# Kernel optimization log

Hardware: AMD Instinct MI355X
Metric: run time of the kernel (lower is better)

Reference implementation:

```python
import jax, jax.numpy as jnp
import numpy as np

HIDDEN = 1024
HEADS = 16
HEAD_DIM = HIDDEN // HEADS  # 64
RP_DIM = 256
KERNEL_EPS = 1e-3


def _gaussian_orthogonal_matrix(nb_rows, nb_cols, seed=0):
    """Orthogonal random features (scaling=0), as in Performer FAVOR+."""
    rng = np.random.RandomState(seed)
    blocks = []
    n_full = nb_rows // nb_cols
    for _ in range(n_full):
        q, _ = np.linalg.qr(rng.randn(nb_cols, nb_cols))
        blocks.append(q.T)
    rem = nb_rows - n_full * nb_cols
    if rem > 0:
        q, _ = np.linalg.qr(rng.randn(nb_cols, nb_cols))
        blocks.append(q.T[:rem])
    mat = np.concatenate(blocks, axis=0)
    # scaling=0: row norms drawn from chi distribution (norms of gaussian rows)
    multiplier = np.linalg.norm(rng.randn(nb_rows, nb_cols), axis=1)
    return (multiplier[:, None] * mat).astype(np.float32)


def setup_inputs() -> dict:
    key = jax.random.key(0)
    kx, kw = jax.random.split(key)
    x = jax.random.normal(kx, (4, 4096, HIDDEN), dtype=jnp.float32)
    w_qkv = jax.random.normal(kw, (HIDDEN, 3 * HIDDEN), dtype=jnp.float32) * 0.02
    b_qkv = jnp.zeros((3 * HIDDEN,), dtype=jnp.float32)
    proj = jnp.asarray(_gaussian_orthogonal_matrix(RP_DIM, HEAD_DIM))  # [M, Dh]
    return {"x": x, "w_qkv": w_qkv, "b_qkv": b_qkv, "proj": proj}


def reference(x, w_qkv, b_qkv, proj):
    B, N, _ = x.shape
    qkv = x @ w_qkv + b_qkv  # [B, N, 3*hidden]
    q, k, v = jnp.split(qkv, 3, axis=-1)

    def to_heads(t):
        return t.reshape(B, N, HEADS, HEAD_DIM).transpose(0, 2, 1, 3)  # bhnd

    q, k, v = to_heads(q), to_heads(k), to_heads(v)

    # forward scales by d**-0.25, generalized_kernel normalizes by d**-0.25 again
    scale = HEAD_DIM ** -0.5
    # generalized kernel features: relu(x_norm @ proj^T) + eps  -> [B,H,N,M]
    q_prime = jax.nn.relu(jnp.einsum('bhnd,md->bhnm', q * scale, proj)) + KERNEL_EPS
    k_prime = jax.nn.relu(jnp.einsum('bhnd,md->bhnm', k * scale, proj)) + KERNEL_EPS

    # non-causal linear attention
    k_sum = k_prime.sum(axis=2)  # [B,H,M]
    d_inv = 1.0 / jnp.einsum('bhnm,bhm->bhn', q_prime, k_sum)  # [B,H,N]
    context = jnp.einsum('bhnm,bhnd->bhmd', k_prime, v)  # [B,H,M,Dh]
    out = jnp.einsum('bhmd,bhnm,bhn->bhnd', context, q_prime, d_inv)

    out = out.transpose(0, 2, 1, 3).reshape(B, N, HIDDEN)
    return out
```

## Files before the change

kernel.cpp:

```cpp
#include <hip/hip_runtime.h>

#define B_   4
#define N_   4096
#define NH   16
#define DH   64
#define HID  1024
#define NC3  3072
#define M_   256
#define BH   64
#define SCALE 0.125f
#define EPS   1e-3f
#define CH2  8
#define CH3  8

typedef _Float16 half8  __attribute__((ext_vector_type(8)));
typedef _Float16 half4v __attribute__((ext_vector_type(4)));
typedef float floatx4   __attribute__((ext_vector_type(4)));

#define GLD_LDS16(gptr, lds_base) \
  __builtin_amdgcn_global_load_lds((const __attribute__((address_space(1))) void*)(gptr), \
                                   (__attribute__((address_space(3))) void*)(lds_base), 16, 0, 0)

#define SBAR() asm volatile("s_barrier" ::: "memory")

__global__ __launch_bounds__(256) void convert_xh(
    const float* __restrict__ x, _Float16* __restrict__ xh,
    const float* __restrict__ proj, _Float16* __restrict__ projh)
{
    if (blockIdx.x >= 8192) {
        const int i = (blockIdx.x - 8192) * 256 + threadIdx.x;
        projh[i] = (_Float16)proj[i];
        return;
    }
    const size_t i = ((size_t)blockIdx.x * 256 + threadIdx.x) * 8;
    float4 a = *(const float4*)(x + i);
    float4 b = *(const float4*)(x + i + 4);
    half8 h;
    h[0] = (_Float16)a.x; h[1] = (_Float16)a.y; h[2] = (_Float16)a.z; h[3] = (_Float16)a.w;
    h[4] = (_Float16)b.x; h[5] = (_Float16)b.y; h[6] = (_Float16)b.z; h[7] = (_Float16)b.w;
    *(half8*)(xh + i) = h;
}

__global__ __launch_bounds__(256) void convert_wT(
    const float* __restrict__ w, _Float16* __restrict__ wT)
{
    __shared__ float t[64][65];
    const int tid = threadIdx.x;
    const int kb = blockIdx.y * 64, nb = blockIdx.x * 64;
    const int c = tid & 63, r0 = tid >> 6;
#pragma unroll
    for (int rr = 0; rr < 64; rr += 4)
        t[rr + r0][c] = w[(size_t)(kb + rr + r0) * NC3 + nb + c];
    __syncthreads();
    const float sc = (nb < 2048) ? SCALE : 1.0f;
#pragma unroll
    for (int rr = 0; rr < 64; rr += 4)
        wT[(size_t)(nb + rr + r0) * HID + kb + c] = (_Float16)(t[c][rr + r0] * sc);
}

__device__ __forceinline__ void stage_tile_qkv(
    const _Float16* __restrict__ xh, const _Float16* __restrict__ wT,
    int row0, int col0, int kt, char* ab, char* bb, int wv, int srow, int sblk)
{
    const size_t ko = (size_t)kt * 64;
#pragma unroll
    for (int s = 0; s < 4; ++s) {
        const int r = s * 64 + srow;
        GLD_LDS16(xh + (size_t)(row0 + r) * HID + ko + 8 * sblk, ab + s * 8192 + wv * 1024);
        GLD_LDS16(wT + (size_t)(col0 + r) * HID + ko + 8 * sblk, bb + s * 8192 + wv * 1024);
    }
}

__global__ __launch_bounds__(512, 2) void gemm_qkv_mfma(
    const _Float16* __restrict__ xh, const _Float16* __restrict__ wT,
    const float* __restrict__ bias,
    _Float16* __restrict__ qh, _Float16* __restrict__ kh, _Float16* __restrict__ vTh)
{
    __shared__ __align__(16) char smem[131072];

    const int tid  = threadIdx.x;
    const int lane = tid & 63;
    const int wv   = tid >> 6;
    const int wm   = wv >> 2;
    const int wn   = wv & 3;
    const int lr   = lane & 15;
    const int lg   = lane >> 4;
    const int lr7  = lr & 7;

    const int bid  = blockIdx.x;
    const int tile = ((bid & 7) * 96) + (bid >> 3);
    const int tm   = tile / 12;
    const int tn   = tile - tm * 12;
    const int row0 = tm * 256;
    const int col0 = tn * 256;

    const int srow = 8 * wv + (lane >> 3);
    const int sblk = (lane & 7) ^ (lane >> 3);

    char* buf0A = smem;
    char* buf0B = smem + 32768;
    char* buf1A = smem + 65536;
    char* buf1B = smem + 98304;

    floatx4 acc[8][4] = {};

    stage_tile_qkv(xh, wT, row0, col0, 0, buf0A, buf0B, wv, srow, sblk);
    stage_tile_qkv(xh, wT, row0, col0, 1, buf1A, buf1B, wv, srow, sblk);

    for (int t = 0; t < 16; ++t) {
        if (t < 15) asm volatile("s_waitcnt vmcnt(8)" ::: "memory");
        else        asm volatile("s_waitcnt vmcnt(0)" ::: "memory");
        SBAR();

        char* ab = (t & 1) ? buf1A : buf0A;
        char* bb = (t & 1) ? buf1B : buf0B;

        half8 a0[8], b0[4];
#pragma unroll
        for (int i = 0; i < 8; ++i)
            a0[i] = *(const half8*)(ab + (wm * 128 + 16 * i + lr) * 128 + ((lg ^ lr7) * 16));
#pragma unroll
        for (int j = 0; j < 4; ++j)
            b0[j] = *(const half8*)(bb + (wn * 64 + 16 * j + lr) * 128 + ((lg ^ lr7) * 16));

        __builtin_amdgcn_s_setprio(1);
#pragma unroll
        for (int i = 0; i < 8; ++i)
#pragma unroll
            for (int j = 0; j < 4; ++j)
                acc[i][j] = __builtin_amdgcn_mfma_f32_16x16x32_f16(a0[i], b0[j], acc[i][j], 0, 0, 0);
        __builtin_amdgcn_s_setprio(0);

        half8 a1[8], b1[4];
#pragma unroll
        for (int i = 0; i < 8; ++i)
            a1[i] = *(const half8*)(ab + (wm * 128 + 16 * i + lr) * 128 + (((4 + lg) ^ lr7) * 16));
#pragma unroll
        for (int j = 0; j < 4; ++j)
            b1[j] = *(const half8*)(bb + (wn * 64 + 16 * j + lr) * 128 + (((4 + lg) ^ lr7) * 16));

        asm volatile("s_waitcnt lgkmcnt(0)" ::: "memory");
        SBAR();
        if (t < 14)
            stage_tile_qkv(xh, wT, row0, col0, t + 2, ab, bb, wv, srow, sblk);

        __builtin_amdgcn_s_setprio(1);
#pragma unroll
        for (int i = 0; i < 8; ++i)
#pragma unroll
            for (int j = 0; j < 4; ++j)
                acc[i][j] = __builtin_amdgcn_mfma_f32_16x16x32_f16(a1[i], b1[j], acc[i][j], 0, 0, 0);
        __builtin_amdgcn_s_setprio(0);
    }

    const int which = col0 >> 10;
    if (which == 2) {
#pragma unroll
        for (int j = 0; j < 4; ++j) {
            const int col = col0 + wn * 64 + 16 * j + lr;
            const int h = (col >> 6) & 15;
            const int d = col & 63;
            const float bb2 = bias[col];
#pragma unroll
            for (int i = 0; i < 8; ++i) {
                const int m0 = row0 + wm * 128 + 16 * i + 4 * lg;
                const int bi = m0 >> 12, n0 = m0 & (N_ - 1);
                half4v hv;
#pragma unroll
                for (int rg = 0; rg < 4; ++rg) hv[rg] = (_Float16)(acc[i][j][rg] + bb2);
                *(half4v*)(vTh + ((size_t)(bi * NH + h) * DH + d) * N_ + n0) = hv;
            }
        }
    } else {
        _Float16* dst = (which == 0) ? qh : kh;
        const int h = ((col0 + wn * 64) >> 6) & 15;
        char* slab = smem + wv * 16384;
#pragma unroll
        for (int i = 0; i < 8; ++i)
#pragma unroll
            for (int j = 0; j < 4; ++j) {
                const float bb2 = bias[col0 + wn * 64 + 16 * j + lr] * SCALE;
                const int d  = 16 * j + lr;
#pragma unroll
                for (int rg = 0; rg < 4; ++rg) {
                    const int nl = 16 * i + 4 * lg + rg;
                    const int pb = (d >> 3) ^ (nl & 7);
                    *(_Float16*)(slab + nl * 128 + pb * 16 + (d & 7) * 2) =
                        (_Float16)(acc[i][j][rg] + bb2);
                }
            }
#pragma unroll
        for (int it = 0; it < 16; ++it) {
            const int nl = it * 8 + (lane >> 3);
            const int pb = (lane & 7) ^ (nl & 7);
            half8 v8 = *(const half8*)(slab + nl * 128 + pb * 16);
            const int m = row0 + wm * 128 + nl;
            const int bi = m >> 12, n = m & (N_ - 1);
            *(half8*)(dst + ((size_t)(bi * NH + h) * N_ + n) * DH + (lane & 7) * 8) = v8;
        }
    }
}

__global__ __launch_bounds__(256) void kv_ctx_mfma(
    const _Float16* __restrict__ kh, const _Float16* __restrict__ vTh,
    const _Float16* __restrict__ projh,
    float* __restrict__ ctx_part, float* __restrict__ ksum_part)
{
    __shared__ __align__(16) _Float16 Kt[64 * 64];
    __shared__ __align__(16) _Float16 Vt[64 * 64];
    __shared__ __align__(16) _Float16 Sp[256 * 64];

    const int tid  = threadIdx.x;
    const int lane = tid & 63;
    const int wv   = tid >> 6;
    const int lr = lane & 15, lg = lane >> 4;
    const int bh = blockIdx.y, chunk = blockIdx.x;
    const int n_base = chunk * (N_ / CH2);

    half8 bfP[4][2];
#pragma unroll
    for (int j = 0; j < 4; ++j)
#pragma unroll
        for (int ks = 0; ks < 2; ++ks)
            bfP[j][ks] = *(const half8*)(projh + (size_t)(64 * wv + 16 * j + lr) * DH + 32 * ks + 8 * lg);

    floatx4 cacc[4][4] = {};
    float ks_acc[4] = {0.f, 0.f, 0.f, 0.f};

    for (int t = 0; t < (N_ / CH2) / 64; ++t) {
        const int n0 = n_base + t * 64;
        __syncthreads();
#pragma unroll
        for (int s = 0; s < 2; ++s) {
            const int R = wv * 16 + s * 8;
            const int r = R + (lane >> 3);
            const int db = (lane & 7) ^ (r & 7);
            GLD_LDS16(kh + ((size_t)(bh * N_ + n0 + r)) * DH + db * 8, (char*)Kt + R * 128);
        }
#pragma unroll
        for (int s = 0; s < 2; ++s) {
            const int R = wv * 16 + s * 8;
            const int r = R + (lane >> 3);
            const int db = (lane & 7) ^ (r & 7);
            GLD_LDS16(vTh + ((size_t)(bh * DH + r)) * N_ + n0 + db * 8, (char*)Vt + R * 128);
        }
        __syncthreads();

        floatx4 s[4][4] = {};
#pragma unroll
        for (int ks = 0; ks < 2; ++ks) {
            half8 aK[4];
#pragma unroll
            for (int i = 0; i < 4; ++i) {
                const int r = 16 * i + lr;
                aK[i] = *(const half8*)((const char*)Kt + r * 128 + (((4 * ks + lg) ^ (r & 7)) * 16));
            }
#pragma unroll
            for (int i = 0; i < 4; ++i)
#pragma unroll
                for (int j = 0; j < 4; ++j)
                    s[i][j] = __builtin_amdgcn_mfma_f32_16x16x32_f16(aK[i], bfP[j][ks], s[i][j], 0, 0, 0);
        }
#pragma unroll
        for (int i = 0; i < 4; ++i)
#pragma unroll
            for (int j = 0; j < 4; ++j) {
                const int m = 64 * wv + 16 * j + lr;
                const int nn0 = 16 * i + 4 * lg;
                half4v h4;
#pragma unroll
                for (int rg = 0; rg < 4; ++rg) {
                    const float kv = fmaxf(s[i][j][rg], 0.f) + EPS;
                    ks_acc[j] += kv;
                    h4[rg] = (_Float16)kv;
                }
                const int db = nn0 >> 3, sub = nn0 & 7;
                *(half4v*)((char*)Sp + m * 128 + ((db ^ (m & 7)) * 16) + sub * 2) = h4;
            }
#pragma unroll
        for (int ks = 0; ks < 2; ++ks) {
            half8 aV[4], bS[4];
#pragma unroll
            for (int i = 0; i < 4; ++i) {
                const int r = 16 * i + lr;
                aV[i] = *(const half8*)((const char*)Vt + r * 128 + (((4 * ks + lg) ^ (r & 7)) * 16));
            }
#pragma unroll
            for (int j = 0; j < 4; ++j) {
                const int m = 64 * wv + 16 * j + lr;
                bS[j] = *(const half8*)((const char*)Sp + m * 128 + (((4 * ks + lg) ^ (m & 7)) * 16));
            }
#pragma unroll
            for (int i = 0; i < 4; ++i)
#pragma unroll
                for (int j = 0; j < 4; ++j)
                    cacc[i][j] = __builtin_amdgcn_mfma_f32_16x16x32_f16(aV[i], bS[j], cacc[i][j], 0, 0, 0);
        }
    }

#pragma unroll
    for (int i = 0; i < 4; ++i)
#pragma unroll
        for (int j = 0; j < 4; ++j)
#pragma unroll
            for (int rg = 0; rg < 4; ++rg) {
                const int d = 16 * i + 4 * lg + rg;
                const int m = 64 * wv + 16 * j + lr;
                ctx_part[(((size_t)chunk * BH + bh) * DH + d) * M_ + m] = cacc[i][j][rg];
            }
#pragma unroll
    for (int j = 0; j < 4; ++j) {
        float v = ks_acc[j];
        v += __shfl_xor(v, 16);
        v += __shfl_xor(v, 32);
        if (lg == 0)
            ksum_part[((size_t)chunk * BH + bh) * M_ + 64 * wv + 16 * j + lr] = v;
    }
}

__global__ __launch_bounds__(256) void reduce_ctx(
    const float* __restrict__ ctx_part, const float* __restrict__ ksum_part,
    _Float16* __restrict__ ctxTh, _Float16* __restrict__ ksumh)
{
    const int idx = blockIdx.x * 256 + threadIdx.x;
    const int CTX = BH * DH * M_;
    if (idx < CTX) {
        float sum = 0.f;
#pragma unroll
        for (int c = 0; c < CH2; ++c) sum += ctx_part[(size_t)c * CTX + idx];
        ctxTh[idx] = (_Float16)sum;
    } else {
        const int kidx = idx - CTX;
        if (kidx < BH * M_) {
            float sum = 0.f;
#pragma unroll
            for (int c = 0; c < CH2; ++c) sum += ksum_part[(size_t)c * BH * M_ + kidx];
            ksumh[kidx] = (_Float16)sum;
        }
    }
}

__global__ __launch_bounds__(256) void attn_out_mfma(
    const _Float16* __restrict__ qh, const _Float16* __restrict__ projh,
    const _Float16* __restrict__ ctxTh, const _Float16* __restrict__ ksumh,
    float* __restrict__ out)
{
    __shared__ __align__(16) _Float16 Ct[64 * 256];
    __shared__ __align__(16) _Float16 Sp[64 * 256];

    const int tid  = threadIdx.x;
    const int lane = tid & 63;
    const int wv   = tid >> 6;
    const int lr = lane & 15, lg = lane >> 4;
    const int bh = blockIdx.y;
    const int bi = bh >> 4, h = bh & 15;
    const int n_base = blockIdx.x * (N_ / CH3);

    {
        const int r_ = (wv << 1) + (lane >> 5);
        const int p_ = lane & 31;
#pragma unroll
        for (int s = 0; s < 8; ++s) {
            const int r = s * 8 + r_;
            const int lb = p_ ^ (r & 31);
            GLD_LDS16(ctxTh + ((size_t)bh * DH + r) * M_ + lb * 8,
                      (char*)Ct + s * 4096 + wv * 1024);
        }
    }

    half8 afP[4][2];
#pragma unroll
    for (int I = 0; I < 4; ++I)
#pragma unroll
        for (int ks = 0; ks < 2; ++ks)
            afP[I][ks] = *(const half8*)(projh + (size_t)(64 * wv + 16 * I + lr) * DH + 32 * ks + 8 * lg);

    for (int t = 0; t < (N_ / CH3) / 64; ++t) {
        const int n0 = n_base + t * 64;
        __syncthreads();
        floatx4 sacc[4][4] = {};
#pragma unroll
        for (int ks = 0; ks < 2; ++ks) {
            half8 bq[4];
#pragma unroll
            for (int J = 0; J < 4; ++J)
                bq[J] = *(const half8*)(qh + ((size_t)bh * N_ + n0 + 16 * J + lr) * DH + 32 * ks + 8 * lg);
#pragma unroll
            for (int I = 0; I < 4; ++I)
#pragma unroll
                for (int J = 0; J < 4; ++J)
                    sacc[I][J] = __builtin_amdgcn_mfma_f32_16x16x32_f16(afP[I][ks], bq[J], sacc[I][J], 0, 0, 0);
        }
#pragma unroll
        for (int I = 0; I < 4; ++I)
#pragma unroll
            for (int J = 0; J < 4; ++J) {
                const int n = 16 * J + lr;
                const int m0 = 64 * wv + 16 * I + 4 * lg;
                half4v h4;
#pragma unroll
                for (int rg = 0; rg < 4; ++rg)
                    h4[rg] = (_Float16)(fmaxf(sacc[I][J][rg], 0.f) + EPS);
                const int db = m0 >> 3, sub = m0 & 7;
                *(half4v*)((char*)Sp + n * 512 + ((db ^ (n & 31)) * 16) + sub * 2) = h4;
            }
        __syncthreads();
        floatx4 oacc[4] = {};
        floatx4 dacc = {};
        const int nl = 16 * wv + lr;
#pragma unroll
        for (int ks = 0; ks < 8; ++ks) {
            half8 aq = *(const half8*)((const char*)Sp + nl * 512 + (((4 * ks + lg) ^ (nl & 31)) * 16));
#pragma unroll
            for (int j = 0; j < 4; ++j) {
                const int d = 16 * j + lr;
                const int pb = (4 * ks + lg) ^ (d & 31);
                half8 bc = *(const half8*)((const char*)Ct + d * 512 + pb * 16);
                oacc[j] = __builtin_amdgcn_mfma_f32_16x16x32_f16(aq, bc, oacc[j], 0, 0, 0);
            }
            half8 bk = {};
            if (lr == 0)
                bk = *(const half8*)(ksumh + (size_t)bh * M_ + 32 * ks + 8 * lg);
            dacc = __builtin_amdgcn_mfma_f32_16x16x32_f16(aq, bk, dacc, 0, 0, 0);
        }
#pragma unroll
        for (int rg = 0; rg < 4; ++rg) {
            float den = dacc[rg];
            den = __shfl(den, lane & 48);
            const float dinv = 1.f / den;
            const int n = n0 + 16 * wv + 4 * lg + rg;
#pragma unroll
            for (int j = 0; j < 4; ++j)
                out[(((size_t)bi * N_ + n) * NH + h) * DH + 16 * j + lr] = oacc[j][rg] * dinv;
        }
    }
}

extern "C" void kernel_launch(void* const* d_in, const int* in_sizes, int n_in,
                              void* d_out, int out_size, void* d_ws, size_t ws_size,
                              hipStream_t stream) {
    const float* x    = (const float*)d_in[0];
    const float* w    = (const float*)d_in[1];
    const float* bias = (const float*)d_in[2];
    const float* proj = (const float*)d_in[3];
    float* out = (float*)d_out;
    char* ws = (char*)d_ws;

    const size_t XN  = (size_t)B_ * N_ * HID;
    const size_t QKV = (size_t)BH * N_ * DH;
    const size_t CTX = (size_t)BH * DH * M_;

    _Float16* xh       = (_Float16*)ws;                          ws += XN * 2;
    _Float16* wT       = (_Float16*)ws;                          ws += NC3 * HID * 2;
    _Float16* projh    = (_Float16*)ws;                          ws += M_ * DH * 2;
    _Float16* qh       = (_Float16*)ws;                          ws += QKV * 2;
    _Float16* kh       = (_Float16*)ws;                          ws += QKV * 2;
    _Float16* vTh      = (_Float16*)ws;                          ws += QKV * 2;
    _Float16* ctxTh    = (_Float16*)ws;                          ws += CTX * 2;
    _Float16* ksumh    = (_Float16*)ws;                          ws += BH * M_ * 2;
    float*    ctx_part = (float*)ws;                             ws += (size_t)CH2 * CTX * 4;
    float*    ksum_part= (float*)ws;                             ws += (size_t)CH2 * BH * M_ * 4;

    convert_xh<<<dim3(XN / (256 * 8) + 64), 256, 0, stream>>>(x, xh, proj, projh);
    convert_wT<<<dim3(NC3 / 64, HID / 64), 256, 0, stream>>>(w, wT);

    gemm_qkv_mfma<<<dim3(768), dim3(512), 0, stream>>>(xh, wT, bias, qh, kh, vTh);

    kv_ctx_mfma<<<dim3(CH2, BH), 256, 0, stream>>>(kh, vTh, projh, ctx_part, ksum_part);

    reduce_ctx<<<dim3((CTX + BH * M_ + 255) / 256), 256, 0, stream>>>(ctx_part, ksum_part, ctxTh, ksumh);

    attn_out_mfma<<<dim3(CH3, BH), 256, 0, stream>>>(qh, projh, ctxTh, ksumh, out);
}
```

Baseline: 314.9 us.

## Split QKV GEMM K-step into quarter phases and hoist k_sum fragment loads

The QKV projection main loop now loads A fragments in halves of four rows instead of eight, reusing one small register set across four MFMA phases separated by barriers. This cuts the fragment registers held live per wave and interleaves LDS reads with MFMA work, at the cost of extra s_barrier points and more LDS read rounds. In the output kernel, the k_sum B-fragments for the denominator MFMA are loaded once into registers before the N loop instead of from global memory in every inner step.

```diff
diff --git a/kernel.cpp b/kernel.cpp
--- a/kernel.cpp
+++ b/kernel.cpp
@@ -115,41 +115,63 @@
         char* ab = (t & 1) ? buf1A : buf0A;
         char* bb = (t & 1) ? buf1B : buf0B;
 
-        half8 a0[8], b0[4];
-#pragma unroll
-        for (int i = 0; i < 8; ++i)
-            a0[i] = *(const half8*)(ab + (wm * 128 + 16 * i + lr) * 128 + ((lg ^ lr7) * 16));
+        half8 af[4], bf[4];
+
+#pragma unroll
+        for (int i = 0; i < 4; ++i)
+            af[i] = *(const half8*)(ab + (wm * 128 + 16 * i + lr) * 128 + ((lg ^ lr7) * 16));
 #pragma unroll
         for (int j = 0; j < 4; ++j)
-            b0[j] = *(const half8*)(bb + (wn * 64 + 16 * j + lr) * 128 + ((lg ^ lr7) * 16));
-
+            bf[j] = *(const half8*)(bb + (wn * 64 + 16 * j + lr) * 128 + ((lg ^ lr7) * 16));
         __builtin_amdgcn_s_setprio(1);
 #pragma unroll
-        for (int i = 0; i < 8; ++i)
+        for (int i = 0; i < 4; ++i)
 #pragma unroll
             for (int j = 0; j < 4; ++j)
-                acc[i][j] = __builtin_amdgcn_mfma_f32_16x16x32_f16(a0[i], b0[j], acc[i][j], 0, 0, 0);
+                acc[i][j] = __builtin_amdgcn_mfma_f32_16x16x32_f16(af[i], bf[j], acc[i][j], 0, 0, 0);
         __builtin_amdgcn_s_setprio(0);
-
-        half8 a1[8], b1[4];
-#pragma unroll
-        for (int i = 0; i < 8; ++i)
-            a1[i] = *(const half8*)(ab + (wm * 128 + 16 * i + lr) * 128 + (((4 + lg) ^ lr7) * 16));
+        SBAR();
+
+#pragma unroll
+        for (int i = 0; i < 4; ++i)
+            af[i] = *(const half8*)(ab + (wm * 128 + 16 * (4 + i) + lr) * 128 + ((lg ^ lr7) * 16));
+        __builtin_amdgcn_s_setprio(1);
+#pragma unroll
+        for (int i = 0; i < 4; ++i)
+#pragma unroll
+            for (int j = 0; j < 4; ++j)
+                acc[4 + i][j] = __builtin_amdgcn_mfma_f32_16x16x32_f16(af[i], bf[j], acc[4 + i][j], 0, 0, 0);
+        __builtin_amdgcn_s_setprio(0);
+        SBAR();
+
+#pragma unroll
+        for (int i = 0; i < 4; ++i)
+            af[i] = *(const half8*)(ab + (wm * 128 + 16 * i + lr) * 128 + (((4 + lg) ^ lr7) * 16));
 #pragma unroll
         for (int j = 0; j < 4; ++j)
-            b1[j] = *(const half8*)(bb + (wn * 64 + 16 * j + lr) * 128 + (((4 + lg) ^ lr7) * 16));
-
+            bf[j] = *(const half8*)(bb + (wn * 64 + 16 * j + lr) * 128 + (((4 + lg) ^ lr7) * 16));
+        __builtin_amdgcn_s_setprio(1);
+#pragma unroll
+        for (int i = 0; i < 4; ++i)
+#pragma unroll
+            for (int j = 0; j < 4; ++j)
+                acc[i][j] = __builtin_amdgcn_mfma_f32_16x16x32_f16(af[i], bf[j], acc[i][j], 0, 0, 0);
+        __builtin_amdgcn_s_setprio(0);
+        SBAR();
+
+#pragma unroll
+        for (int i = 0; i < 4; ++i)
+            af[i] = *(const half8*)(ab + (wm * 128 + 16 * (4 + i) + lr) * 128 + (((4 + lg) ^ lr7) * 16));
         asm volatile("s_waitcnt lgkmcnt(0)" ::: "memory");
         SBAR();
         if (t < 14)
             stage_tile_qkv(xh, wT, row0, col0, t + 2, ab, bb, wv, srow, sblk);
-
         __builtin_amdgcn_s_setprio(1);
 #pragma unroll
-        for (int i = 0; i < 8; ++i)
+        for (int i = 0; i < 4; ++i)
 #pragma unroll
             for (int j = 0; j < 4; ++j)
-                acc[i][j] = __builtin_amdgcn_mfma_f32_16x16x32_f16(a1[i], b1[j], acc[i][j], 0, 0, 0);
+                acc[4 + i][j] = __builtin_amdgcn_mfma_f32_16x16x32_f16(af[i], bf[j], acc[4 + i][j], 0, 0, 0);
         __builtin_amdgcn_s_setprio(0);
     }
 
@@ -375,6 +397,13 @@
         for (int ks = 0; ks < 2; ++ks)
             afP[I][ks] = *(const half8*)(projh + (size_t)(64 * wv + 16 * I + lr) * DH + 32 * ks + 8 * lg);
 
+    half8 bk8[8] = {};
+    if (lr == 0) {
+#pragma unroll
+        for (int ks = 0; ks < 8; ++ks)
+            bk8[ks] = *(const half8*)(ksumh + (size_t)bh * M_ + 32 * ks + 8 * lg);
+    }
+
     for (int t = 0; t < (N_ / CH3) / 64; ++t) {
         const int n0 = n_base + t * 64;
         __syncthreads();
@@ -418,10 +447,7 @@
                 half8 bc = *(const half8*)((const char*)Ct + d * 512 + pb * 16);
                 oacc[j] = __builtin_amdgcn_mfma_f32_16x16x32_f16(aq, bc, oacc[j], 0, 0, 0);
             }
-            half8 bk = {};
-            if (lr == 0)
-                bk = *(const half8*)(ksumh + (size_t)bh * M_ + 32 * ks + 8 * lg);
-            dacc = __builtin_amdgcn_mfma_f32_16x16x32_f16(aq, bk, dacc, 0, 0, 0);
+            dacc = __builtin_amdgcn_mfma_f32_16x16x32_f16(aq, bk8[ks], dacc, 0, 0, 0);
         }
 #pragma unroll
         for (int rg = 0; rg < 4; ++rg) {
```

After: 326.6 us. +3.7%, slower.

## Double-buffer K/V staging in kv_ctx kernel and hoist ksum loads

Applied to the files above, without the earlier changes.

The K/V tile loads in the context kernel now go into two LDS buffers, with the next-but-one tile prefetched through async global-to-LDS loads gated by explicit vmcnt waits. This lets memory latency overlap the MFMA work instead of stalling at a sync every iteration. All K and V fragments are read into registers up front so the buffer can be refilled early. Separately, the ksum fragments in the output kernel are loaded once before the loop rather than on every iteration. The cost is more LDS and more registers, which may reduce occupancy.

```diff
diff --git a/kernel.cpp b/kernel.cpp
--- a/kernel.cpp
+++ b/kernel.cpp
@@ -201,13 +201,31 @@
     }
 }
 
+__device__ __forceinline__ void stage_kv(
+    const _Float16* __restrict__ kh, const _Float16* __restrict__ vTh,
+    int bh, int n0, char* ktb, char* vtb, int wv, int r8_, int db_)
+{
+#pragma unroll
+    for (int s = 0; s < 2; ++s) {
+        const int R = wv * 16 + s * 8;
+        const int r = R + r8_;
+        GLD_LDS16(kh + ((size_t)(bh * N_ + n0 + r)) * DH + db_ * 8, ktb + R * 128);
+    }
+#pragma unroll
+    for (int s = 0; s < 2; ++s) {
+        const int R = wv * 16 + s * 8;
+        const int r = R + r8_;
+        GLD_LDS16(vTh + ((size_t)(bh * DH + r)) * N_ + n0 + db_ * 8, vtb + R * 128);
+    }
+}
+
 __global__ __launch_bounds__(256) void kv_ctx_mfma(
     const _Float16* __restrict__ kh, const _Float16* __restrict__ vTh,
     const _Float16* __restrict__ projh,
     float* __restrict__ ctx_part, float* __restrict__ ksum_part)
 {
-    __shared__ __align__(16) _Float16 Kt[64 * 64];
-    __shared__ __align__(16) _Float16 Vt[64 * 64];
+    __shared__ __align__(16) _Float16 Kt[2][64 * 64];
+    __shared__ __align__(16) _Float16 Vt[2][64 * 64];
     __shared__ __align__(16) _Float16 Sp[256 * 64];
 
     const int tid  = threadIdx.x;
@@ -216,6 +234,10 @@
     const int lr = lane & 15, lg = lane >> 4;
     const int bh = blockIdx.y, chunk = blockIdx.x;
     const int n_base = chunk * (N_ / CH2);
+    const int NT = (N_ / CH2) / 64;
+
+    const int r8_ = lane >> 3;
+    const int db_ = (lane & 7) ^ r8_;
 
     half8 bfP[4][2];
 #pragma unroll
@@ -227,40 +249,43 @@
     floatx4 cacc[4][4] = {};
     float ks_acc[4] = {0.f, 0.f, 0.f, 0.f};
 
-    for (int t = 0; t < (N_ / CH2) / 64; ++t) {
-        const int n0 = n_base + t * 64;
-        __syncthreads();
-#pragma unroll
-        for (int s = 0; s < 2; ++s) {
-            const int R = wv * 16 + s * 8;
-            const int r = R + (lane >> 3);
-            const int db = (lane & 7) ^ (r & 7);
-            GLD_LDS16(kh + ((size_t)(bh * N_ + n0 + r)) * DH + db * 8, (char*)Kt + R * 128);
-        }
-#pragma unroll
-        for (int s = 0; s < 2; ++s) {
-            const int R = wv * 16 + s * 8;
-            const int r = R + (lane >> 3);
-            const int db = (lane & 7) ^ (r & 7);
-            GLD_LDS16(vTh + ((size_t)(bh * DH + r)) * N_ + n0 + db * 8, (char*)Vt + R * 128);
-        }
-        __syncthreads();
-
-        floatx4 s[4][4] = {};
-#pragma unroll
-        for (int ks = 0; ks < 2; ++ks) {
-            half8 aK[4];
+    stage_kv(kh, vTh, bh, n_base,      (char*)Kt[0], (char*)Vt[0], wv, r8_, db_);
+    stage_kv(kh, vTh, bh, n_base + 64, (char*)Kt[1], (char*)Vt[1], wv, r8_, db_);
+
+    for (int t = 0; t < NT; ++t) {
+        if (t < NT - 1) asm volatile("s_waitcnt vmcnt(4)" ::: "memory");
+        else            asm volatile("s_waitcnt vmcnt(0)" ::: "memory");
+        SBAR();
+
+        const int b = t & 1;
+        const char* KtB = (const char*)Kt[b];
+        const char* VtB = (const char*)Vt[b];
+
+        half8 aK[2][4], aV[2][4];
+#pragma unroll
+        for (int ks = 0; ks < 2; ++ks)
 #pragma unroll
             for (int i = 0; i < 4; ++i) {
                 const int r = 16 * i + lr;
-                aK[i] = *(const half8*)((const char*)Kt + r * 128 + (((4 * ks + lg) ^ (r & 7)) * 16));
-            }
+                const int po = ((4 * ks + lg) ^ (r & 7)) * 16;
+                aK[ks][i] = *(const half8*)(KtB + r * 128 + po);
+                aV[ks][i] = *(const half8*)(VtB + r * 128 + po);
+            }
+        asm volatile("s_waitcnt lgkmcnt(0)" ::: "memory");
+        SBAR();
+        if (t + 2 < NT)
+            stage_kv(kh, vTh, bh, n_base + (t + 2) * 64,
+                     (char*)Kt[b], (char*)Vt[b], wv, r8_, db_);
+
+        floatx4 s[4][4] = {};
+#pragma unroll
+        for (int ks = 0; ks < 2; ++ks)
 #pragma unroll
             for (int i = 0; i < 4; ++i)
 #pragma unroll
                 for (int j = 0; j < 4; ++j)
-                    s[i][j] = __builtin_amdgcn_mfma_f32_16x16x32_f16(aK[i], bfP[j][ks], s[i][j], 0, 0, 0);
-        }
+                    s[i][j] = __builtin_amdgcn_mfma_f32_16x16x32_f16(aK[ks][i], bfP[j][ks], s[i][j], 0, 0, 0);
+
 #pragma unroll
         for (int i = 0; i < 4; ++i)
 #pragma unroll
@@ -277,14 +302,10 @@
                 const int db = nn0 >> 3, sub = nn0 & 7;
                 *(half4v*)((char*)Sp + m * 128 + ((db ^ (m & 7)) * 16) + sub * 2) = h4;
             }
+
 #pragma unroll
         for (int ks = 0; ks < 2; ++ks) {
-            half8 aV[4], bS[4];
-#pragma unroll
-            for (int i = 0; i < 4; ++i) {
-                const int r = 16 * i + lr;
-                aV[i] = *(const half8*)((const char*)Vt + r * 128 + (((4 * ks + lg) ^ (r & 7)) * 16));
-            }
+            half8 bS[4];
 #pragma unroll
             for (int j = 0; j < 4; ++j) {
                 const int m = 64 * wv + 16 * j + lr;
@@ -294,7 +315,7 @@
             for (int i = 0; i < 4; ++i)
 #pragma unroll
                 for (int j = 0; j < 4; ++j)
-                    cacc[i][j] = __builtin_amdgcn_mfma_f32_16x16x32_f16(aV[i], bS[j], cacc[i][j], 0, 0, 0);
+                    cacc[i][j] = __builtin_amdgcn_mfma_f32_16x16x32_f16(aV[ks][i], bS[j], cacc[i][j], 0, 0, 0);
         }
     }
 
@@ -375,6 +396,13 @@
         for (int ks = 0; ks < 2; ++ks)
             afP[I][ks] = *(const half8*)(projh + (size_t)(64 * wv + 16 * I + lr) * DH + 32 * ks + 8 * lg);
 
+    half8 bk8[8] = {};
+    if (lr == 0) {
+#pragma unroll
+        for (int ks = 0; ks < 8; ++ks)
+            bk8[ks] = *(const half8*)(ksumh + (size_t)bh * M_ + 32 * ks + 8 * lg);
+    }
+
     for (int t = 0; t < (N_ / CH3) / 64; ++t) {
         const int n0 = n_base + t * 64;
         __syncthreads();
@@ -418,10 +446,7 @@
                 half8 bc = *(const half8*)((const char*)Ct + d * 512 + pb * 16);
                 oacc[j] = __builtin_amdgcn_mfma_f32_16x16x32_f16(aq, bc, oacc[j], 0, 0, 0);
             }
-            half8 bk = {};
-            if (lr == 0)
-                bk = *(const half8*)(ksumh + (size_t)bh * M_ + 32 * ks + 8 * lg);
-            dacc = __builtin_amdgcn_mfma_f32_16x16x32_f16(aq, bk, dacc, 0, 0, 0);
+            dacc = __builtin_amdgcn_mfma_f32_16x16x32_f16(aq, bk8[ks], dacc, 0, 0, 0);
         }
 #pragma unroll
         for (int rg = 0; rg < 4; ++rg) {
```

After: 335.3 us. +6.5%, slower.
